# Kernel optimization log

Measured on AMD Instinct MI355X. Metric: run time of the kernel, lower is better.

Reference implementation:

```python
import jax, jax.numpy as jnp
import numpy as np

B, D, H = 8192, 256, 64


def setup_inputs() -> dict:
    key = jax.random.key(0)
    ks = jax.random.split(key, 7)
    noise = jax.random.normal(ks[0], (B, D), dtype=jnp.float32)
    adj_logits = jax.random.normal(ks[1], (D, D), dtype=jnp.float32) * 0.1
    # stacked per-node mechanism params: Linear(D,H) -> SiLU -> Linear(H,1)
    W1 = jax.random.normal(ks[2], (D, H, D), dtype=jnp.float32) * (1.0 / np.sqrt(D))
    b1 = jax.random.normal(ks[3], (D, H), dtype=jnp.float32) * (1.0 / np.sqrt(D))
    W2 = jax.random.normal(ks[4], (D, H), dtype=jnp.float32) * (1.0 / np.sqrt(H))
    b2 = jax.random.normal(ks[5], (D,), dtype=jnp.float32) * (1.0 / np.sqrt(H))
    log_sigma = jnp.zeros((D,), dtype=jnp.float32)  # torch init: tensor(0.0)
    return {"noise": noise, "adj_logits": adj_logits, "W1": W1, "b1": b1,
            "W2": W2, "b2": b2, "log_sigma": log_sigma}


def reference(noise, adj_logits, W1, b1, W2, b2, log_sigma):
    d = adj_logits.shape[0]
    # differentiable adjacency: sigmoid(logits) with zeroed diagonal
    adj = jax.nn.sigmoid(adj_logits) * (1.0 - jnp.eye(d, dtype=adj_logits.dtype))
    bsz = noise.shape[0]
    z0 = jnp.zeros((bsz, d), dtype=noise.dtype)

    def step(z, xs):
        i, a_col, w1, bb1, w2, bb2, ls, n_i = xs
        pv = z * a_col[None, :]                       # [B, D] masked parent values
        h = jax.nn.silu(pv @ w1.T + bb1[None, :])     # [B, H]
        det = h @ w2 + bb2                            # [B]
        val = det + jnp.exp(ls) * n_i                 # [B]
        z = jax.lax.dynamic_update_slice(z, val[:, None], (0, i))
        return z, None

    xs = (jnp.arange(d), adj.T, W1, b1, W2, b2, log_sigma, noise.T)
    z, _ = jax.lax.scan(step, z0, xs)
    return z
```

## Files before the change

kernel.cpp:

```cpp
#include <hip/hip_runtime.h>
#include <math.h>

#define Dn 256
#define Hn 64

typedef __attribute__((ext_vector_type(8))) short short8;
typedef __attribute__((ext_vector_type(4))) float floatx4;
typedef __attribute__((ext_vector_type(4))) unsigned int uint4v;

#define PIN(x) asm volatile("" :: "v"(x))

static __device__ __forceinline__ unsigned short f2bf(float x) {
    unsigned int u = __float_as_uint(x);
    unsigned int r = (u + 0x7fffu + ((u >> 16) & 1u)) >> 16;
    return (unsigned short)r;
}

__global__ __launch_bounds__(256) void prep_sgm(const float* __restrict__ adj,
                                                float* __restrict__ sgm) {
    const int i = blockIdx.x, j = threadIdx.x;
    float m = 0.f;
    if (j != i) m = 1.f / (1.f + __expf(-adj[(size_t)j * Dn + i]));
    sgm[(size_t)i * Dn + j] = m;
}

__global__ __launch_bounds__(256) void prep_wb(const float* __restrict__ W1,
                                               const float* __restrict__ sgm,
                                               unsigned short* __restrict__ Wb) {
    const int c = blockIdx.x, i = blockIdx.y;
    const int t = threadIdx.x;
    const int nb = t >> 6, l = t & 63;
    const int kk = nb * 16 + (l & 15);
    const int jb = c * 32 + ((l >> 4) & 3) * 8;
    const float* wp = W1 + ((size_t)i * Hn + kk) * Dn + jb;
    const float* sp = sgm + (size_t)i * Dn + jb;
    unsigned short v[8];
#pragma unroll
    for (int e = 0; e < 8; ++e) v[e] = f2bf(wp[e] * sp[e]);
    unsigned short* dst = Wb + ((((size_t)i * 8 + c) * 4 + nb) * 64 + l) * 8;
    *(short8*)dst = *(const short8*)v;
}

__global__ __launch_bounds__(256) void prep_nst(const float* __restrict__ noise,
                                                const float* __restrict__ ls,
                                                float* __restrict__ nsT, int B) {
    __shared__ float tile[64][65];
    const int bi = blockIdx.x * 64, dj = blockIdx.y * 64;
    const int t = threadIdx.x, c = t & 63, rq = t >> 6;
#pragma unroll
    for (int it = 0; it < 16; ++it) {
        int b = bi + it * 4 + rq;
        tile[it * 4 + rq][c] = noise[(size_t)b * Dn + dj + c];
    }
    __syncthreads();
#pragma unroll
    for (int it = 0; it < 16; ++it) {
        int d = dj + it * 4 + rq;
        float sg = __expf(ls[d]);
        nsT[(size_t)d * B + bi + c] = tile[c][it * 4 + rq] * sg;
    }
}

__global__ __launch_bounds__(128, 1) void scm_main(const unsigned short* __restrict__ Wb,
                                                   const float* __restrict__ b1,
                                                   const float* __restrict__ W2,
                                                   const float* __restrict__ b2,
                                                   const float* __restrict__ nsT,
                                                   float* __restrict__ out, int B) {
    const int t = threadIdx.x;
    const int w = t >> 6, l = t & 63;
    const int n = l & 15, q = l >> 4;
    const int rowbase = blockIdx.x * 32 + w * 16;

    const unsigned short* wb_l = Wb + (size_t)l * 8;

    short8 af[8];
    short8 wf[8][4];
    uint4v ain = {0u, 0u, 0u, 0u};
    floatx4 b1v[4], w2v[4];
    float nvv, b2v;

#pragma unroll
    for (int nb = 0; nb < 4; ++nb) {
        b1v[nb] = *(const floatx4*)(b1 + nb * 16 + q * 4);
        w2v[nb] = *(const floatx4*)(W2 + nb * 16 + q * 4);
    }
    nvv = nsT[rowbase + n];
    b2v = b2[0];

#pragma unroll
    for (int sec = 0; sec < 8; ++sec) {
        if (sec > 0) {
            af[sec - 1] = __builtin_bit_cast(short8, ain);
            ain = (uint4v){0u, 0u, 0u, 0u};
        }
#pragma unroll 1
        for (int ii = 0; ii < 32; ++ii) {
            const int i = sec * 32 + ii;

            floatx4 aA[4], aB[4];
#pragma unroll
            for (int nb = 0; nb < 4; ++nb) {
                aA[nb] = (floatx4){0.f, 0.f, 0.f, 0.f};
                aB[nb] = (floatx4){0.f, 0.f, 0.f, 0.f};
            }

            if (ii != 0) {
                short8 zi = __builtin_bit_cast(short8, ain);
#pragma unroll
                for (int nb = 0; nb < 4; ++nb)
                    aB[nb] = __builtin_amdgcn_mfma_f32_16x16x32_bf16(wf[sec][nb], zi, aB[nb], 0, 0, 0);
            }
#pragma unroll
            for (int c = 0; c < 8; ++c)
                if (c < sec) {
#pragma unroll
                    for (int nb = 0; nb < 4; ++nb)
                        aA[nb] = __builtin_amdgcn_mfma_f32_16x16x32_bf16(wf[c][nb], af[c], aA[nb], 0, 0, 0);
                }

            floatx4 b1c[4], w2c[4];
            float nvc = nvv, b2c = b2v;
#pragma unroll
            for (int nb = 0; nb < 4; ++nb) { b1c[nb] = b1v[nb]; w2c[nb] = w2v[nb]; }

            {
                int ip = i + 1; if (ip > 255) ip = 255;
                const unsigned short* wp = wb_l + (size_t)ip * 16384;
#pragma unroll
                for (int c = 0; c < 8; ++c)
                    if (c <= sec) {
#pragma unroll
                        for (int nb = 0; nb < 4; ++nb)
                            wf[c][nb] = *(const short8*)(wp + c * 2048 + nb * 512);
                    }
#pragma unroll
                for (int nb = 0; nb < 4; ++nb) {
                    b1v[nb] = *(const floatx4*)(b1 + ip * Hn + nb * 16 + q * 4);
                    w2v[nb] = *(const floatx4*)(W2 + ip * Hn + nb * 16 + q * 4);
                }
                nvv = nsT[(size_t)ip * B + rowbase + n];
                b2v = b2[ip];
            }

            float s = 0.f;
#pragma unroll
            for (int nb = 0; nb < 4; ++nb) {
#pragma unroll
                for (int r = 0; r < 4; ++r) {
                    float h = (aA[nb][r] + aB[nb][r]) + b1c[nb][r];
                    s += __fdividef(h, 1.f + __expf(-h)) * w2c[nb][r];
                }
            }
            s += __shfl_xor(s, 16);
            s += __shfl_xor(s, 32);
            float z = s + b2c + nvc;

            {
                unsigned int zb = (unsigned int)f2bf(z);
                unsigned int sh = (unsigned int)(ii & 1) << 4;
                unsigned int val = zb << sh;
                unsigned int msk = 0xFFFFu << sh;
                const int own = (q == (ii >> 3));
                const int wsel = (ii >> 1) & 3;
#pragma unroll
                for (int wd = 0; wd < 4; ++wd) {
                    unsigned int merged = (ain[wd] & ~msk) | val;
                    ain[wd] = (own && (wsel == wd)) ? merged : ain[wd];
                }
            }

            if (q == 0) out[(size_t)(rowbase + n) * Dn + i] = z;

#pragma unroll
            for (int c = 0; c < 8; ++c)
                if (c <= sec) {
#pragma unroll
                    for (int nb = 0; nb < 4; ++nb) PIN(wf[c][nb]);
                }
#pragma unroll
            for (int nb = 0; nb < 4; ++nb) { PIN(b1v[nb]); PIN(w2v[nb]); }
            PIN(nvv); PIN(b2v);
        }
    }
}

extern "C" void kernel_launch(void* const* d_in, const int* in_sizes, int n_in,
                              void* d_out, int out_size, void* d_ws, size_t ws_size,
                              hipStream_t stream) {
    const float* noise      = (const float*)d_in[0];
    const float* adj_logits = (const float*)d_in[1];
    const float* W1         = (const float*)d_in[2];
    const float* b1         = (const float*)d_in[3];
    const float* W2         = (const float*)d_in[4];
    const float* b2         = (const float*)d_in[5];
    const float* log_sigma  = (const float*)d_in[6];
    float* out = (float*)d_out;

    const int B = in_sizes[0] / Dn;
    unsigned short* Wb  = (unsigned short*)d_ws;
    float*          nsT = (float*)((char*)d_ws + (size_t)Dn * Dn * Hn * 2);
    float*          sgm = nsT;

    prep_sgm<<<dim3(Dn), 256, 0, stream>>>(adj_logits, sgm);
    prep_wb<<<dim3(8, Dn), 256, 0, stream>>>(W1, sgm, Wb);
    prep_nst<<<dim3(B / 64, Dn / 64), 256, 0, stream>>>(noise, log_sigma, nsT, B);
    scm_main<<<dim3(B / 32), 128, 0, stream>>>(Wb, b1, W2, b2, nsT, out, B);
}
```

Baseline: 402.2 us.

## Prefetch per-node weights via global_load_lds double-buffered LDS ring

Replaces register-held prefetch of the next node's bf16 W1 fragments, b1, W2, noise and b2 with direct global-to-LDS async loads into a two-slot ring per wave, reading operands back from LDS for the MFMAs. This frees a large block of VGPRs that previously held weight fragments and pinning asm. The inner loop is also unrolled by 8 so output z values are gathered and written as two float4 stores instead of scalar stores. It adds LDS read traffic and a full vmcnt(0) wait each step, which could serialize the prefetch against compute.

```diff
diff --git a/kernel.cpp b/kernel.cpp
--- a/kernel.cpp
+++ b/kernel.cpp
@@ -7,13 +7,22 @@
 typedef __attribute__((ext_vector_type(8))) short short8;
 typedef __attribute__((ext_vector_type(4))) float floatx4;
 typedef __attribute__((ext_vector_type(4))) unsigned int uint4v;
-
-#define PIN(x) asm volatile("" :: "v"(x))
 
 static __device__ __forceinline__ unsigned short f2bf(float x) {
     unsigned int u = __float_as_uint(x);
     unsigned int r = (u + 0x7fffu + ((u >> 16) & 1u)) >> 16;
     return (unsigned short)r;
+}
+
+static __device__ __forceinline__ void gll16(const unsigned short* g, unsigned short* l) {
+    __builtin_amdgcn_global_load_lds(
+        (const __attribute__((address_space(1))) unsigned int*)g,
+        (__attribute__((address_space(3))) unsigned int*)l, 16, 0, 0);
+}
+static __device__ __forceinline__ void gll4(const float* g, float* l) {
+    __builtin_amdgcn_global_load_lds(
+        (const __attribute__((address_space(1))) unsigned int*)g,
+        (__attribute__((address_space(3))) unsigned int*)l, 4, 0, 0);
 }
 
 __global__ __launch_bounds__(256) void prep_sgm(const float* __restrict__ adj,
@@ -67,26 +76,22 @@
                                                    const float* __restrict__ b2,
                                                    const float* __restrict__ nsT,
                                                    float* __restrict__ out, int B) {
+    __shared__ __align__(16) unsigned short ring[2][2][8][4][512];
+    __shared__ __align__(16) float sring[2][2][256];
+
     const int t = threadIdx.x;
     const int w = t >> 6, l = t & 63;
     const int n = l & 15, q = l >> 4;
     const int rowbase = blockIdx.x * 32 + w * 16;
 
-    const unsigned short* wb_l = Wb + (size_t)l * 8;
-
     short8 af[8];
-    short8 wf[8][4];
     uint4v ain = {0u, 0u, 0u, 0u};
-    floatx4 b1v[4], w2v[4];
-    float nvv, b2v;
-
-#pragma unroll
-    for (int nb = 0; nb < 4; ++nb) {
-        b1v[nb] = *(const floatx4*)(b1 + nb * 16 + q * 4);
-        w2v[nb] = *(const floatx4*)(W2 + nb * 16 + q * 4);
-    }
-    nvv = nsT[rowbase + n];
-    b2v = b2[0];
+    const floatx4 zf4 = {0.f, 0.f, 0.f, 0.f};
+
+    gll4(b1 + l,            &sring[0][w][0]);
+    gll4(W2 + l,            &sring[0][w][64]);
+    gll4(nsT + rowbase + n, &sring[0][w][128]);
+    gll4(b2,                &sring[0][w][192]);
 
 #pragma unroll
     for (int sec = 0; sec < 8; ++sec) {
@@ -95,92 +100,99 @@
             ain = (uint4v){0u, 0u, 0u, 0u};
         }
 #pragma unroll 1
-        for (int ii = 0; ii < 32; ++ii) {
-            const int i = sec * 32 + ii;
-
-            floatx4 aA[4], aB[4];
-#pragma unroll
-            for (int nb = 0; nb < 4; ++nb) {
-                aA[nb] = (floatx4){0.f, 0.f, 0.f, 0.f};
-                aB[nb] = (floatx4){0.f, 0.f, 0.f, 0.f};
+        for (int ii8 = 0; ii8 < 4; ++ii8) {
+            float zz[8];
+#pragma unroll
+            for (int e8 = 0; e8 < 8; ++e8) {
+                const int ii = ii8 * 8 + e8;
+                const int i  = sec * 32 + ii;
+                const int sl = e8 & 1;
+                const int ns = sl ^ 1;
+
+                asm volatile("s_waitcnt vmcnt(0)" ::: "memory");
+                __builtin_amdgcn_sched_barrier(0);
+
+                if (i < 255) {
+                    const int ip = i + 1;
+                    const unsigned short* wrow = Wb + (size_t)ip * 16384 + (size_t)l * 8;
+#pragma unroll
+                    for (int c = 0; c < 8; ++c)
+                        if (c <= sec) {
+#pragma unroll
+                            for (int nb = 0; nb < 4; ++nb)
+                                gll16(wrow + c * 2048 + nb * 512, &ring[ns][w][c][nb][0]);
+                        }
+                    gll4(b1 + ip * Hn + l,                   &sring[ns][w][0]);
+                    gll4(W2 + ip * Hn + l,                   &sring[ns][w][64]);
+                    gll4(nsT + (size_t)ip * B + rowbase + n, &sring[ns][w][128]);
+                    gll4(b2 + ip,                            &sring[ns][w][192]);
+                }
+                __builtin_amdgcn_sched_barrier(0);
+
+                floatx4 b1c[4], w2c[4];
+#pragma unroll
+                for (int nb = 0; nb < 4; ++nb) {
+                    b1c[nb] = *(const floatx4*)&sring[sl][w][nb * 16 + q * 4];
+                    w2c[nb] = *(const floatx4*)&sring[sl][w][64 + nb * 16 + q * 4];
+                }
+                const float nvc = sring[sl][w][128 + n];
+                const float b2c = sring[sl][w][192];
+
+                floatx4 aA[4], aB4[4];
+#pragma unroll
+                for (int nb = 0; nb < 4; ++nb) { aA[nb] = zf4; aB4[nb] = zf4; }
+
+                if (ii != 0) {
+                    short8 zi = __builtin_bit_cast(short8, ain);
+#pragma unroll
+                    for (int nb = 0; nb < 4; ++nb) {
+                        short8 wfs = *(const short8*)&ring[sl][w][sec][nb][(size_t)l * 8];
+                        aB4[nb] = __builtin_amdgcn_mfma_f32_16x16x32_bf16(wfs, zi, aB4[nb], 0, 0, 0);
+                    }
+                }
+#pragma unroll
+                for (int c = 0; c < 8; ++c)
+                    if (c < sec) {
+#pragma unroll
+                        for (int nb = 0; nb < 4; ++nb) {
+                            short8 wfc = *(const short8*)&ring[sl][w][c][nb][(size_t)l * 8];
+                            aA[nb] = __builtin_amdgcn_mfma_f32_16x16x32_bf16(wfc, af[c], aA[nb], 0, 0, 0);
+                        }
+                    }
+
+                float ssum = 0.f;
+#pragma unroll
+                for (int nb = 0; nb < 4; ++nb) {
+#pragma unroll
+                    for (int r = 0; r < 4; ++r) {
+                        float h = (aA[nb][r] + aB4[nb][r]) + b1c[nb][r];
+                        ssum += __fdividef(h, 1.f + __expf(-h)) * w2c[nb][r];
+                    }
+                }
+                ssum += __shfl_xor(ssum, 16);
+                ssum += __shfl_xor(ssum, 32);
+                const float z_ = ssum + b2c + nvc;
+
+                {
+                    unsigned int zb = ((unsigned int)f2bf(z_)) << (16 * (e8 & 1));
+                    const unsigned int msk = 0xFFFFu << (16 * (e8 & 1));
+                    const int own = (q == ii8);
+                    const int wsel = (e8 >> 1) & 3;
+#pragma unroll
+                    for (int wd = 0; wd < 4; ++wd) {
+                        unsigned int mg = (ain[wd] & ~msk) | zb;
+                        ain[wd] = (own && (wsel == wd)) ? mg : ain[wd];
+                    }
+                }
+                zz[e8] = z_;
             }
-
-            if (ii != 0) {
-                short8 zi = __builtin_bit_cast(short8, ain);
-#pragma unroll
-                for (int nb = 0; nb < 4; ++nb)
-                    aB[nb] = __builtin_amdgcn_mfma_f32_16x16x32_bf16(wf[sec][nb], zi, aB[nb], 0, 0, 0);
+            if (q == 0) {
+                float* op = out + (size_t)(rowbase + n) * Dn + sec * 32 + ii8 * 8;
+                floatx4 o0 = {zz[0], zz[1], zz[2], zz[3]};
+                floatx4 o1 = {zz[4], zz[5], zz[6], zz[7]};
+                *(floatx4*)(op)     = o0;
+                *(floatx4*)(op + 4) = o1;
             }
-#pragma unroll
-            for (int c = 0; c < 8; ++c)
-                if (c < sec) {
-#pragma unroll
-                    for (int nb = 0; nb < 4; ++nb)
-                        aA[nb] = __builtin_amdgcn_mfma_f32_16x16x32_bf16(wf[c][nb], af[c], aA[nb], 0, 0, 0);
-                }
-
-            floatx4 b1c[4], w2c[4];
-            float nvc = nvv, b2c = b2v;
-#pragma unroll
-            for (int nb = 0; nb < 4; ++nb) { b1c[nb] = b1v[nb]; w2c[nb] = w2v[nb]; }
-
-            {
-                int ip = i + 1; if (ip > 255) ip = 255;
-                const unsigned short* wp = wb_l + (size_t)ip * 16384;
-#pragma unroll
-                for (int c = 0; c < 8; ++c)
-                    if (c <= sec) {
-#pragma unroll
-                        for (int nb = 0; nb < 4; ++nb)
-                            wf[c][nb] = *(const short8*)(wp + c * 2048 + nb * 512);
-                    }
-#pragma unroll
-                for (int nb = 0; nb < 4; ++nb) {
-                    b1v[nb] = *(const floatx4*)(b1 + ip * Hn + nb * 16 + q * 4);
-                    w2v[nb] = *(const floatx4*)(W2 + ip * Hn + nb * 16 + q * 4);
-                }
-                nvv = nsT[(size_t)ip * B + rowbase + n];
-                b2v = b2[ip];
-            }
-
-            float s = 0.f;
-#pragma unroll
-            for (int nb = 0; nb < 4; ++nb) {
-#pragma unroll
-                for (int r = 0; r < 4; ++r) {
-                    float h = (aA[nb][r] + aB[nb][r]) + b1c[nb][r];
-                    s += __fdividef(h, 1.f + __expf(-h)) * w2c[nb][r];
-                }
-            }
-            s += __shfl_xor(s, 16);
-            s += __shfl_xor(s, 32);
-            float z = s + b2c + nvc;
-
-            {
-                unsigned int zb = (unsigned int)f2bf(z);
-                unsigned int sh = (unsigned int)(ii & 1) << 4;
-                unsigned int val = zb << sh;
-                unsigned int msk = 0xFFFFu << sh;
-                const int own = (q == (ii >> 3));
-                const int wsel = (ii >> 1) & 3;
-#pragma unroll
-                for (int wd = 0; wd < 4; ++wd) {
-                    unsigned int merged = (ain[wd] & ~msk) | val;
-                    ain[wd] = (own && (wsel == wd)) ? merged : ain[wd];
-                }
-            }
-
-            if (q == 0) out[(size_t)(rowbase + n) * Dn + i] = z;
-
-#pragma unroll
-            for (int c = 0; c < 8; ++c)
-                if (c <= sec) {
-#pragma unroll
-                    for (int nb = 0; nb < 4; ++nb) PIN(wf[c][nb]);
-                }
-#pragma unroll
-            for (int nb = 0; nb < 4; ++nb) { PIN(b1v[nb]); PIN(w2v[nb]); }
-            PIN(nvv); PIN(b2v);
         }
     }
 }
```

Measured after the change: 559.1 us. 39.0% more time.
